# Kernel optimization log

Hardware: AMD Instinct MI355X
Metric: run time of the kernel (lower is better)

## Reference

```python
import jax, jax.numpy as jnp
import numpy as np

EMBED_DIM = 256
NUM_HEADS = 8
NB = 8          # number of scenes (batches)
LQ = 256        # queries per scene
LS = 4096       # source points per scene
LN_EPS = 1e-5


def setup_inputs() -> dict:
    key = jax.random.key(0)
    ks = jax.random.split(key, 8)
    d = EMBED_DIM
    n_q, n_s = NB * LQ, NB * LS
    w_scale = d ** -0.5  # xavier-ish
    return {
        "source": jax.random.normal(ks[0], (n_s, d), jnp.float32),
        "query": jax.random.normal(ks[1], (n_q, d), jnp.float32),
        "source_pe": 0.1 * jax.random.normal(ks[2], (n_s, d), jnp.float32),
        "query_pe": 0.1 * jax.random.normal(ks[3], (n_q, d), jnp.float32),
        "in_proj_w": w_scale * jax.random.normal(ks[4], (3 * d, d), jnp.float32),
        "in_proj_b": jnp.zeros((3 * d,), jnp.float32),
        "out_w": w_scale * jax.random.normal(ks[5], (d, d), jnp.float32),
        "out_b": jnp.zeros((d,), jnp.float32),
        "ln_w": jnp.ones((d,), jnp.float32),
        "ln_b": jnp.zeros((d,), jnp.float32),
        # sorted equal-size segments: token i belongs to scene i // L
        "source_batch": (jnp.arange(n_s, dtype=jnp.int32) // LS).astype(jnp.int32),
        "query_batch": (jnp.arange(n_q, dtype=jnp.int32) // LQ).astype(jnp.int32),
        "B": NB,
    }


def reference(source, query, source_pe, query_pe, in_proj_w, in_proj_b,
              out_w, out_b, ln_w, ln_b, source_batch, query_batch, B):
    d = source.shape[-1]
    H = NUM_HEADS
    hd = d // H
    Lq = query.shape[0] // B
    Ls = source.shape[0] // B

    # batch ids are sorted equal segments -> per-scene gather == reshape
    q_in = (query + query_pe).reshape(B, Lq, d)   # q with pos embed
    k_in = (source + source_pe).reshape(B, Ls, d) # k with pos embed
    v_in = source.reshape(B, Ls, d)               # v without pos embed

    Wq, Wk, Wv = jnp.split(in_proj_w, 3, axis=0)
    bq, bk, bv = jnp.split(in_proj_b, 3)

    q = (q_in @ Wq.T + bq).reshape(B, Lq, H, hd)
    k = (k_in @ Wk.T + bk).reshape(B, Ls, H, hd)
    v = (v_in @ Wv.T + bv).reshape(B, Ls, H, hd)

    scores = jnp.einsum('bqhd,bkhd->bhqk', q, k) * (hd ** -0.5)
    attn = jax.nn.softmax(scores, axis=-1)
    o = jnp.einsum('bhqk,bkhd->bqhd', attn, v).reshape(B, Lq, d)
    o = o @ out_w.T + out_b

    # residual (dropout is identity at p=0) + LayerNorm
    res = o + query.reshape(B, Lq, d)
    mu = jnp.mean(res, axis=-1, keepdims=True)
    var = jnp.var(res, axis=-1, keepdims=True)
    y = (res - mu) * jax.lax.rsqrt(var + LN_EPS) * ln_w + ln_b
    return y.reshape(-1, d)
```

## Files before the change

### kernel.cpp

```cpp
#include <hip/hip_runtime.h>
#include <hip/hip_bf16.h>

typedef __bf16 bf16;
typedef __bf16 bf16x4 __attribute__((ext_vector_type(4)));
typedef __bf16 bf16x8 __attribute__((ext_vector_type(8)));
typedef float f32x4 __attribute__((ext_vector_type(4)));

#define D 256
#define NHEAD 8
#define HD 32
#define NB_ 8
#define LQ_ 256
#define LS_ 4096
#define MQ (NB_ * LQ_)
#define MS (NB_ * LS_)

#define QSCALE 0.25500527f

__global__ __launch_bounds__(256) void prep(
    const float* __restrict__ source, const float* __restrict__ source_pe,
    const float* __restrict__ query, const float* __restrict__ query_pe,
    const float* __restrict__ w_in, const float* __restrict__ w_out,
    bf16* __restrict__ SPb, bf16* __restrict__ Sb, bf16* __restrict__ QPb,
    bf16* __restrict__ Wb, int write_sb)
{
    const int NS4 = MS * D / 4;
    const int NQ4 = MQ * D / 4;
    const int NW4 = (768 * 256 + 256 * 256) / 4;
    const int total = NS4 + NQ4 + NW4;
    for (int i = blockIdx.x * 256 + threadIdx.x; i < total; i += gridDim.x * 256) {
        if (i < NS4) {
            const float4 s = ((const float4*)source)[i];
            const float4 p = ((const float4*)source_pe)[i];
            bf16x4 osp;
            osp[0] = (bf16)(s.x + p.x); osp[1] = (bf16)(s.y + p.y);
            osp[2] = (bf16)(s.z + p.z); osp[3] = (bf16)(s.w + p.w);
            ((bf16x4*)SPb)[i] = osp;
            if (write_sb) {
                bf16x4 os;
                os[0] = (bf16)s.x; os[1] = (bf16)s.y;
                os[2] = (bf16)s.z; os[3] = (bf16)s.w;
                ((bf16x4*)Sb)[i] = os;
            }
        } else if (i < NS4 + NQ4) {
            const int j = i - NS4;
            const float4 s = ((const float4*)query)[j];
            const float4 p = ((const float4*)query_pe)[j];
            bf16x4 o;
            o[0] = (bf16)(s.x + p.x); o[1] = (bf16)(s.y + p.y);
            o[2] = (bf16)(s.z + p.z); o[3] = (bf16)(s.w + p.w);
            ((bf16x4*)QPb)[j] = o;
        } else {
            const int j = i - NS4 - NQ4;
            const float4 v = (j < 49152) ? ((const float4*)w_in)[j]
                                         : ((const float4*)w_out)[j - 49152];
            bf16x4 o;
            o[0] = (bf16)v.x; o[1] = (bf16)v.y; o[2] = (bf16)v.z; o[3] = (bf16)v.w;
            ((bf16x4*)Wb)[j] = o;
        }
    }
}

__global__ __launch_bounds__(256) void prep2(
    const float* __restrict__ source, bf16* __restrict__ Sb)
{
    const int NS4 = MS * D / 4;
    for (int i = blockIdx.x * 256 + threadIdx.x; i < NS4; i += gridDim.x * 256) {
        const float4 s = ((const float4*)source)[i];
        bf16x4 o;
        o[0] = (bf16)s.x; o[1] = (bf16)s.y; o[2] = (bf16)s.z; o[3] = (bf16)s.w;
        ((bf16x4*)Sb)[i] = o;
    }
}

__global__ __launch_bounds__(256, 2) void gemm_proj_all(
    const bf16* __restrict__ SPb, const bf16* __restrict__ Sb,
    const bf16* __restrict__ QPb, const bf16* __restrict__ Wb,
    const float* __restrict__ in_proj_b,
    bf16* __restrict__ Kt, bf16* __restrict__ Vt2, bf16* __restrict__ Qb,
    int mode)
{
    __shared__ bf16 As[128][72];
    __shared__ bf16 Bs[256][72];
    const int tid = threadIdx.x, lane = tid & 63, wid = tid >> 6;
    const int wm = wid >> 1, wn = wid & 1;
    const int g = lane >> 4, q15 = lane & 15;
    const int id = blockIdx.x;

    const bf16* A; const bf16* W; const float* bias; bf16* out;
    int omode; int mblk;
    if (mode == 0) {
        if (id < 256)      { A = SPb; W = Wb + 256 * D; bias = in_proj_b + 256; out = Kt;  mblk = id;       omode = 1; }
        else if (id < 512) { A = Sb;  W = Wb + 512 * D; bias = in_proj_b + 512; out = Vt2; mblk = id - 256; omode = 2; }
        else               { A = QPb; W = Wb;           bias = in_proj_b;       out = Qb;  mblk = id - 512; omode = 0; }
    } else if (mode == 1) {
        if (id < 256)      { A = SPb; W = Wb + 256 * D; bias = in_proj_b + 256; out = Kt;  mblk = id;       omode = 1; }
        else               { A = QPb; W = Wb;           bias = in_proj_b;       out = Qb;  mblk = id - 256; omode = 0; }
    } else {
        A = Sb; W = Wb + 512 * D; bias = in_proj_b + 512; out = Vt2; mblk = id; omode = 2;
    }

    f32x4 acc[4][8];
    #pragma unroll
    for (int i = 0; i < 4; ++i)
        #pragma unroll
        for (int j = 0; j < 8; ++j) acc[i][j] = (f32x4){0.f, 0.f, 0.f, 0.f};

    const size_t arow0 = (size_t)mblk * 128;

    for (int kk = 0; kk < 4; ++kk) {
        const int d0 = kk * 64;
        #pragma unroll
        for (int i = 0; i < 4; ++i) {
            const int idx = i * 256 + tid;
            const int r = idx >> 3, c = (idx & 7) * 8;
            *(bf16x8*)&As[r][c] = *(const bf16x8*)&A[(arow0 + r) * D + d0 + c];
        }
        #pragma unroll
        for (int i = 0; i < 8; ++i) {
            const int idx = i * 256 + tid;
            const int r = idx >> 3, c = (idx & 7) * 8;
            *(bf16x8*)&Bs[r][c] = *(const bf16x8*)&W[(size_t)r * D + d0 + c];
        }
        __syncthreads();
        #pragma unroll
        for (int h2 = 0; h2 < 2; ++h2) {
            const int ko = h2 * 32 + g * 8;
            bf16x8 af[4], bfr[8];
            #pragma unroll
            for (int i = 0; i < 4; ++i)
                af[i] = *(const bf16x8*)&As[wm * 64 + i * 16 + q15][ko];
            #pragma unroll
            for (int j = 0; j < 8; ++j)
                bfr[j] = *(const bf16x8*)&Bs[wn * 128 + j * 16 + q15][ko];
            #pragma unroll
            for (int i = 0; i < 4; ++i)
                #pragma unroll
                for (int j = 0; j < 8; ++j)
                    acc[i][j] = __builtin_amdgcn_mfma_f32_16x16x32_bf16(
                        af[i], bfr[j], acc[i][j], 0, 0, 0);
        }
        __syncthreads();
    }

    if (omode == 0) {
        #pragma unroll
        for (int i = 0; i < 4; ++i)
            #pragma unroll
            for (int j = 0; j < 8; ++j) {
                const int n_g = wn * 128 + j * 16 + q15;
                const float b = bias[n_g];
                #pragma unroll
                for (int r = 0; r < 4; ++r) {
                    const size_t m_g = arow0 + wm * 64 + i * 16 + g * 4 + r;
                    out[m_g * D + n_g] = (bf16)((acc[i][j][r] + b) * QSCALE);
                }
            }
    } else if (omode == 1) {
        #pragma unroll
        for (int i = 0; i < 4; ++i)
            #pragma unroll
            for (int j = 0; j < 8; ++j) {
                const int n_g = wn * 128 + j * 16 + q15;
                const int h = n_g >> 5, d = n_g & 31;
                const int gp = d >> 3, e = d & 7;
                const float b = bias[n_g];
                #pragma unroll
                for (int r = 0; r < 4; ++r) {
                    const size_t m_g = arow0 + wm * 64 + i * 16 + g * 4 + r;
                    const int bb = (int)(m_g >> 12);
                    const int c = (int)((m_g & 4095) >> 6);
                    const int kl = (int)(m_g & 63);
                    const int t = ((kl >> 5) << 1) | ((kl >> 2) & 1);
                    const int q15p = ((kl >> 3) & 3) * 4 + (kl & 3);
                    out[((size_t)(bb * 8 + h) * 64 + c) * 2048
                        + t * 512 + (gp * 16 + q15p) * 8 + e] = (bf16)(acc[i][j][r] + b);
                }
            }
    } else {
        #pragma unroll
        for (int i = 0; i < 4; ++i)
            #pragma unroll
            for (int j = 0; j < 8; ++j) {
                const int n_g = wn * 128 + j * 16 + q15;
                const int h = n_g >> 5, d = n_g & 31;
                const int dt = d >> 4, q15p = d & 15;
                const float b = bias[n_g];
                const size_t m_g0 = arow0 + wm * 64 + i * 16 + g * 4;
                const int bb = (int)(m_g0 >> 12);
                const int c = (int)((m_g0 & 4095) >> 6);
                const int kl0 = (int)(m_g0 & 63);
                const int half = kl0 >> 5, gp = (kl0 >> 3) & 3, e0 = kl0 & 7;
                const int f = dt * 2 + half;
                bf16x4 o;
                #pragma unroll
                for (int r = 0; r < 4; ++r) o[r] = (bf16)(acc[i][j][r] + b);
                *(bf16x4*)&out[((size_t)(bb * 8 + h) * 64 + c) * 2048
                               + f * 512 + (gp * 16 + q15p) * 8 + e0] = o;
            }
    }
}

template<int S>
__global__ __launch_bounds__(256, 8) void attn_kernel(
    const bf16* __restrict__ Qb, const bf16* __restrict__ Kt,
    const bf16* __restrict__ Vt2,
    float* __restrict__ accp, float* __restrict__ lp)
{
    const int tid = threadIdx.x, lane = tid & 63, wid = tid >> 6;
    const int q15 = lane & 15, g = lane >> 4;
    const int bid = blockIdx.x;
    const int h = bid & 7;
    const int inner = bid >> 3;
    const int b = inner / (S * 4);
    const int rem = inner % (S * 4);
    const int split = rem >> 2, qt = rem & 3;
    constexpr int CHUNKS = LS_ / S / 64;

    const int q0 = b * LQ_ + qt * 64 + wid * 16;
    const bf16x8 qf = *(const bf16x8*)&Qb[(size_t)(q0 + q15) * D + h * HD + g * 8];

    const f32x4 minit = (f32x4){-8.f, -8.f, -8.f, -8.f};
    const size_t cbase = ((size_t)(b * 8 + h) * 64 + split * CHUNKS) * 2048;
    const bf16* kp = Kt + cbase + lane * 8;
    const bf16* vp = Vt2 + cbase + lane * 8;

    float l_run = 0.f;
    f32x4 acc0 = (f32x4){0.f, 0.f, 0.f, 0.f};
    f32x4 acc1 = (f32x4){0.f, 0.f, 0.f, 0.f};

    for (int kc = 0; kc < CHUNKS; ++kc) {
        const size_t co = (size_t)kc * 2048;

        bf16x8 kf[4], vf[4];
        #pragma unroll
        for (int t = 0; t < 4; ++t) kf[t] = *(const bf16x8*)&kp[co + t * 512];
        #pragma unroll
        for (int f = 0; f < 4; ++f) vf[f] = *(const bf16x8*)&vp[co + f * 512];

        f32x4 s[4];
        #pragma unroll
        for (int t = 0; t < 4; ++t)
            s[t] = __builtin_amdgcn_mfma_f32_16x16x32_bf16(kf[t], qf, minit, 0, 0, 0);

        bf16x8 pa0, pa1;
        #pragma unroll
        for (int r = 0; r < 4; ++r) {
            const float p0 = exp2f(s[0][r]);
            const float p1 = exp2f(s[1][r]);
            const float p2 = exp2f(s[2][r]);
            const float p3 = exp2f(s[3][r]);
            l_run += (p0 + p1) + (p2 + p3);
            pa0[r]     = (bf16)p0;
            pa0[4 + r] = (bf16)p1;
            pa1[r]     = (bf16)p2;
            pa1[4 + r] = (bf16)p3;
        }

        acc0 = __builtin_amdgcn_mfma_f32_16x16x32_bf16(pa0, vf[0], acc0, 0, 0, 0);
        acc0 = __builtin_amdgcn_mfma_f32_16x16x32_bf16(pa1, vf[1], acc0, 0, 0, 0);
        acc1 = __builtin_amdgcn_mfma_f32_16x16x32_bf16(pa0, vf[2], acc1, 0, 0, 0);
        acc1 = __builtin_amdgcn_mfma_f32_16x16x32_bf16(pa1, vf[3], acc1, 0, 0, 0);
    }

    l_run += __shfl_xor(l_run, 16);
    l_run += __shfl_xor(l_run, 32);

    const int task = (b * 8 + h) * 16 + qt * 4 + wid;
    const size_t base = ((size_t)(task * S + split) * 64 + lane) * 8;
    *(f32x4*)&accp[base]     = acc0;
    *(f32x4*)&accp[base + 4] = acc1;
    if (lane < 16)
        lp[(task * S + split) * 16 + lane] = l_run;
}

template<int S>
__global__ __launch_bounds__(256) void attn_combine(
    const float* __restrict__ accp, const float* __restrict__ lp,
    bf16* __restrict__ Ob)
{
    const int tid = threadIdx.x, lane = tid & 63, wid = tid >> 6;
    const int task = blockIdx.x * 4 + wid;
    const int g = lane >> 4, q15 = lane & 15;

    f32x4 o0 = (f32x4){0.f, 0.f, 0.f, 0.f};
    f32x4 o1 = (f32x4){0.f, 0.f, 0.f, 0.f};
    float ll = 0.f;
    #pragma unroll
    for (int s = 0; s < S; ++s) {
        const size_t base = ((size_t)(task * S + s) * 64 + lane) * 8;
        o0 += *(const f32x4*)&accp[base];
        o1 += *(const f32x4*)&accp[base + 4];
        if (lane < 16) ll += lp[(task * S + s) * 16 + lane];
    }

    const int b = task >> 7, h = (task >> 4) & 7, qg = task & 15;
    #pragma unroll
    for (int r = 0; r < 4; ++r) {
        const float inv = 1.f / __shfl(ll, g * 4 + r);
        const size_t row = (size_t)b * LQ_ + qg * 16 + g * 4 + r;
        Ob[row * D + h * HD + q15]      = (bf16)(o0[r] * inv);
        Ob[row * D + h * HD + 16 + q15] = (bf16)(o1[r] * inv);
    }
}

__global__ __launch_bounds__(256) void out_ln_kernel(
    const bf16* __restrict__ Ob, const bf16* __restrict__ Wout,
    const float* __restrict__ out_b, const float* __restrict__ query,
    const float* __restrict__ lnw, const float* __restrict__ lnb,
    float* __restrict__ out)
{
    __shared__ bf16 As[128][72];
    __shared__ bf16 Bs[256][72];
    __shared__ float red[2][128][2];
    const int tid = threadIdx.x, lane = tid & 63, wid = tid >> 6;
    const int wm = wid >> 1, wn = wid & 1;
    const int g = lane >> 4, q15 = lane & 15;
    const int mblk = blockIdx.x;

    f32x4 acc[4][8];
    #pragma unroll
    for (int i = 0; i < 4; ++i)
        #pragma unroll
        for (int j = 0; j < 8; ++j) acc[i][j] = (f32x4){0.f, 0.f, 0.f, 0.f};

    for (int kk = 0; kk < 4; ++kk) {
        const int d0 = kk * 64;
        #pragma unroll
        for (int i = 0; i < 4; ++i) {
            const int idx = i * 256 + tid;
            const int r = idx >> 3, c = (idx & 7) * 8;
            *(bf16x8*)&As[r][c] =
                *(const bf16x8*)&Ob[(size_t)(mblk * 128 + r) * D + d0 + c];
        }
        #pragma unroll
        for (int i = 0; i < 8; ++i) {
            const int idx = i * 256 + tid;
            const int r = idx >> 3, c = (idx & 7) * 8;
            *(bf16x8*)&Bs[r][c] = *(const bf16x8*)&Wout[(size_t)r * D + d0 + c];
        }
        __syncthreads();
        #pragma unroll
        for (int h2 = 0; h2 < 2; ++h2) {
            const int ko = h2 * 32 + g * 8;
            bf16x8 af[4], bfr[8];
            #pragma unroll
            for (int i = 0; i < 4; ++i)
                af[i] = *(const bf16x8*)&As[wm * 64 + i * 16 + q15][ko];
            #pragma unroll
            for (int j = 0; j < 8; ++j)
                bfr[j] = *(const bf16x8*)&Bs[wn * 128 + j * 16 + q15][ko];
            #pragma unroll
            for (int i = 0; i < 4; ++i)
                #pragma unroll
                for (int j = 0; j < 8; ++j)
                    acc[i][j] = __builtin_amdgcn_mfma_f32_16x16x32_bf16(
                        af[i], bfr[j], acc[i][j], 0, 0, 0);
        }
        __syncthreads();
    }

    float bl[8], lw[8], lbv[8];
    #pragma unroll
    for (int j = 0; j < 8; ++j) {
        const int n = wn * 128 + j * 16 + q15;
        bl[j] = out_b[n]; lw[j] = lnw[n]; lbv[j] = lnb[n];
    }

    #pragma unroll
    for (int i = 0; i < 4; ++i) {
        #pragma unroll
        for (int r = 0; r < 4; ++r) {
            const size_t m = (size_t)mblk * 128 + wm * 64 + i * 16 + g * 4 + r;
            float s = 0.f, sq = 0.f;
            #pragma unroll
            for (int j = 0; j < 8; ++j) {
                const float v = acc[i][j][r] + bl[j] + query[m * D + wn * 128 + j * 16 + q15];
                acc[i][j][r] = v;
                s += v; sq += v * v;
            }
            s += __shfl_xor(s, 1);  sq += __shfl_xor(sq, 1);
            s += __shfl_xor(s, 2);  sq += __shfl_xor(sq, 2);
            s += __shfl_xor(s, 4);  sq += __shfl_xor(sq, 4);
            s += __shfl_xor(s, 8);  sq += __shfl_xor(sq, 8);
            if (q15 == i * 4 + r) {
                red[wn][wm * 64 + i * 16 + g * 4 + r][0] = s;
                red[wn][wm * 64 + i * 16 + g * 4 + r][1] = sq;
            }
        }
    }
    __syncthreads();

    #pragma unroll
    for (int i = 0; i < 4; ++i)
        #pragma unroll
        for (int r = 0; r < 4; ++r) {
            const int row = wm * 64 + i * 16 + g * 4 + r;
            const float s  = red[0][row][0] + red[1][row][0];
            const float sq = red[0][row][1] + red[1][row][1];
            const float mean = s * (1.f / 256.f);
            const float var  = sq * (1.f / 256.f) - mean * mean;
            const float inv  = rsqrtf(var + 1e-5f);
            const size_t m = (size_t)mblk * 128 + row;
            #pragma unroll
            for (int j = 0; j < 8; ++j)
                out[m * D + wn * 128 + j * 16 + q15] =
                    (acc[i][j][r] - mean) * inv * lw[j] + lbv[j];
        }
}

extern "C" void kernel_launch(void* const* d_in, const int* in_sizes, int n_in,
                              void* d_out, int out_size, void* d_ws, size_t ws_size,
                              hipStream_t stream) {
    (void)in_sizes; (void)n_in; (void)out_size;
    const float* source    = (const float*)d_in[0];
    const float* query     = (const float*)d_in[1];
    const float* source_pe = (const float*)d_in[2];
    const float* query_pe  = (const float*)d_in[3];
    const float* in_proj_w = (const float*)d_in[4];
    const float* in_proj_b = (const float*)d_in[5];
    const float* out_w     = (const float*)d_in[6];
    const float* out_b     = (const float*)d_in[7];
    const float* ln_w      = (const float*)d_in[8];
    const float* ln_b      = (const float*)d_in[9];

    constexpr int S = 8;
    bf16* Wb  = (bf16*)d_ws;
    bf16* Qb  = Wb + 1024 * 256;
    bf16* Kt  = Qb + (size_t)MQ * D;
    bf16* Vt2 = Kt + (size_t)MS * D;
    bf16* Ob  = Vt2 + (size_t)MS * D;
    bf16* QPb = Ob + (size_t)MQ * D;
    bf16* SPb = QPb + (size_t)MQ * D;
    bf16* Sb  = SPb + (size_t)MS * D;
    float* lp   = (float*)QPb;
    float* outp = (float*)d_out;

    const size_t need_fast = (size_t)((char*)(Sb + (size_t)MS * D) - (char*)d_ws);
    const bool fast = (ws_size >= need_fast);

    if (fast) {
        prep<<<dim3(2048), dim3(256), 0, stream>>>(
            source, source_pe, query, query_pe, in_proj_w, out_w,
            SPb, Sb, QPb, Wb, 1);
        gemm_proj_all<<<dim3(528), dim3(256), 0, stream>>>(
            SPb, Sb, QPb, Wb, in_proj_b, Kt, Vt2, Qb, 0);
        float* accp = (float*)Sb;
        attn_kernel<S><<<dim3(256 * S), dim3(256), 0, stream>>>(Qb, Kt, Vt2, accp, lp);
        attn_combine<S><<<dim3(256), dim3(256), 0, stream>>>(accp, lp, Ob);
    } else {
        prep<<<dim3(2048), dim3(256), 0, stream>>>(
            source, source_pe, query, query_pe, in_proj_w, out_w,
            SPb, SPb, QPb, Wb, 0);
        gemm_proj_all<<<dim3(272), dim3(256), 0, stream>>>(
            SPb, SPb, QPb, Wb, in_proj_b, Kt, Vt2, Qb, 1);
        prep2<<<dim3(2048), dim3(256), 0, stream>>>(source, SPb);
        gemm_proj_all<<<dim3(256), dim3(256), 0, stream>>>(
            SPb, SPb, QPb, Wb, in_proj_b, Kt, Vt2, Qb, 2);
        float* accp = (float*)SPb;
        attn_kernel<S><<<dim3(256 * S), dim3(256), 0, stream>>>(Qb, Kt, Vt2, accp, lp);
        attn_combine<S><<<dim3(256), dim3(256), 0, stream>>>(accp, lp, Ob);
    }

    out_ln_kernel<<<dim3(16), dim3(256), 0, stream>>>(
        Ob, Wb + 768 * 256, out_b, query, ln_w, ln_b, outp);
}
```

Baseline: 94.42 us.

## Fuse fp32-to-bf16 input conversion into projection GEMM; double queries per attention wave

Removes the standalone prep pass that wrote bf16 copies of source+pe, source and query+pe. The projection GEMM now loads fp32 inputs directly, adds the positional embedding and converts to bf16 while filling shared memory. Only the weights are still cast in a small separate kernel. The attention kernel now has each wave handle 32 queries (two 16-row tiles) that share the same K/V fragment loads, halving the grid and lowering the occupancy hint from 8 to 4. This trades extra register pressure and doubled fp32 global reads inside the GEMM for much less intermediate traffic and better K/V reuse.

```diff
diff --git a/kernel.cpp b/kernel.cpp
--- a/kernel.cpp
+++ b/kernel.cpp
@@ -17,68 +17,25 @@
 
 #define QSCALE 0.25500527f
 
-__global__ __launch_bounds__(256) void prep(
+__global__ __launch_bounds__(256) void wcast(
+    const float* __restrict__ w_in, const float* __restrict__ w_out,
+    bf16* __restrict__ wb)
+{
+    const int idx = blockIdx.x * 256 + threadIdx.x;
+    const int n_in4 = (768 * 256) / 4;
+    float4 v;
+    if (idx < n_in4) v = ((const float4*)w_in)[idx];
+    else             v = ((const float4*)w_out)[idx - n_in4];
+    bf16x4 o;
+    o[0] = (bf16)v.x; o[1] = (bf16)v.y; o[2] = (bf16)v.z; o[3] = (bf16)v.w;
+    *(bf16x4*)&wb[(size_t)idx * 4] = o;
+}
+
+__global__ __launch_bounds__(256, 2) void gemm_fused(
     const float* __restrict__ source, const float* __restrict__ source_pe,
     const float* __restrict__ query, const float* __restrict__ query_pe,
-    const float* __restrict__ w_in, const float* __restrict__ w_out,
-    bf16* __restrict__ SPb, bf16* __restrict__ Sb, bf16* __restrict__ QPb,
-    bf16* __restrict__ Wb, int write_sb)
-{
-    const int NS4 = MS * D / 4;
-    const int NQ4 = MQ * D / 4;
-    const int NW4 = (768 * 256 + 256 * 256) / 4;
-    const int total = NS4 + NQ4 + NW4;
-    for (int i = blockIdx.x * 256 + threadIdx.x; i < total; i += gridDim.x * 256) {
-        if (i < NS4) {
-            const float4 s = ((const float4*)source)[i];
-            const float4 p = ((const float4*)source_pe)[i];
-            bf16x4 osp;
-            osp[0] = (bf16)(s.x + p.x); osp[1] = (bf16)(s.y + p.y);
-            osp[2] = (bf16)(s.z + p.z); osp[3] = (bf16)(s.w + p.w);
-            ((bf16x4*)SPb)[i] = osp;
-            if (write_sb) {
-                bf16x4 os;
-                os[0] = (bf16)s.x; os[1] = (bf16)s.y;
-                os[2] = (bf16)s.z; os[3] = (bf16)s.w;
-                ((bf16x4*)Sb)[i] = os;
-            }
-        } else if (i < NS4 + NQ4) {
-            const int j = i - NS4;
-            const float4 s = ((const float4*)query)[j];
-            const float4 p = ((const float4*)query_pe)[j];
-            bf16x4 o;
-            o[0] = (bf16)(s.x + p.x); o[1] = (bf16)(s.y + p.y);
-            o[2] = (bf16)(s.z + p.z); o[3] = (bf16)(s.w + p.w);
-            ((bf16x4*)QPb)[j] = o;
-        } else {
-            const int j = i - NS4 - NQ4;
-            const float4 v = (j < 49152) ? ((const float4*)w_in)[j]
-                                         : ((const float4*)w_out)[j - 49152];
-            bf16x4 o;
-            o[0] = (bf16)v.x; o[1] = (bf16)v.y; o[2] = (bf16)v.z; o[3] = (bf16)v.w;
-            ((bf16x4*)Wb)[j] = o;
-        }
-    }
-}
-
-__global__ __launch_bounds__(256) void prep2(
-    const float* __restrict__ source, bf16* __restrict__ Sb)
-{
-    const int NS4 = MS * D / 4;
-    for (int i = blockIdx.x * 256 + threadIdx.x; i < NS4; i += gridDim.x * 256) {
-        const float4 s = ((const float4*)source)[i];
-        bf16x4 o;
-        o[0] = (bf16)s.x; o[1] = (bf16)s.y; o[2] = (bf16)s.z; o[3] = (bf16)s.w;
-        ((bf16x4*)Sb)[i] = o;
-    }
-}
-
-__global__ __launch_bounds__(256, 2) void gemm_proj_all(
-    const bf16* __restrict__ SPb, const bf16* __restrict__ Sb,
-    const bf16* __restrict__ QPb, const bf16* __restrict__ Wb,
-    const float* __restrict__ in_proj_b,
-    bf16* __restrict__ Kt, bf16* __restrict__ Vt2, bf16* __restrict__ Qb,
-    int mode)
+    const bf16* __restrict__ Wb, const float* __restrict__ in_proj_b,
+    bf16* __restrict__ Kt, bf16* __restrict__ Vt2, bf16* __restrict__ Qb)
 {
     __shared__ bf16 As[128][72];
     __shared__ bf16 Bs[256][72];
@@ -87,17 +44,17 @@
     const int g = lane >> 4, q15 = lane & 15;
     const int id = blockIdx.x;
 
-    const bf16* A; const bf16* W; const float* bias; bf16* out;
+    const float* A; const float* P; const bf16* W; const float* bias; bf16* out;
     int omode; int mblk;
-    if (mode == 0) {
-        if (id < 256)      { A = SPb; W = Wb + 256 * D; bias = in_proj_b + 256; out = Kt;  mblk = id;       omode = 1; }
-        else if (id < 512) { A = Sb;  W = Wb + 512 * D; bias = in_proj_b + 512; out = Vt2; mblk = id - 256; omode = 2; }
-        else               { A = QPb; W = Wb;           bias = in_proj_b;       out = Qb;  mblk = id - 512; omode = 0; }
-    } else if (mode == 1) {
-        if (id < 256)      { A = SPb; W = Wb + 256 * D; bias = in_proj_b + 256; out = Kt;  mblk = id;       omode = 1; }
-        else               { A = QPb; W = Wb;           bias = in_proj_b;       out = Qb;  mblk = id - 256; omode = 0; }
+    if (id < 256) {
+        A = source; P = source_pe; W = Wb + 256 * D; bias = in_proj_b + 256;
+        out = Kt; mblk = id; omode = 1;
+    } else if (id < 512) {
+        A = source; P = nullptr;   W = Wb + 512 * D; bias = in_proj_b + 512;
+        out = Vt2; mblk = id - 256; omode = 2;
     } else {
-        A = Sb; W = Wb + 512 * D; bias = in_proj_b + 512; out = Vt2; mblk = id; omode = 2;
+        A = query;  P = query_pe;  W = Wb;           bias = in_proj_b;
+        out = Qb; mblk = id - 512; omode = 0;
     }
 
     f32x4 acc[4][8];
@@ -111,10 +68,18 @@
     for (int kk = 0; kk < 4; ++kk) {
         const int d0 = kk * 64;
         #pragma unroll
-        for (int i = 0; i < 4; ++i) {
+        for (int i = 0; i < 8; ++i) {
             const int idx = i * 256 + tid;
-            const int r = idx >> 3, c = (idx & 7) * 8;
-            *(bf16x8*)&As[r][c] = *(const bf16x8*)&A[(arow0 + r) * D + d0 + c];
+            const int r = idx >> 4, c = (idx & 15) * 4;
+            const size_t gof = (arow0 + r) * D + d0 + c;
+            float4 v = *(const float4*)&A[gof];
+            if (P) {
+                const float4 p = *(const float4*)&P[gof];
+                v.x += p.x; v.y += p.y; v.z += p.z; v.w += p.w;
+            }
+            bf16x4 o;
+            o[0] = (bf16)v.x; o[1] = (bf16)v.y; o[2] = (bf16)v.z; o[3] = (bf16)v.w;
+            *(bf16x4*)&As[r][c] = o;
         }
         #pragma unroll
         for (int i = 0; i < 8; ++i) {
@@ -202,7 +167,7 @@
 }
 
 template<int S>
-__global__ __launch_bounds__(256, 8) void attn_kernel(
+__global__ __launch_bounds__(256, 4) void attn_kernel(
     const bf16* __restrict__ Qb, const bf16* __restrict__ Kt,
     const bf16* __restrict__ Vt2,
     float* __restrict__ accp, float* __restrict__ lp)
@@ -212,22 +177,26 @@
     const int bid = blockIdx.x;
     const int h = bid & 7;
     const int inner = bid >> 3;
-    const int b = inner / (S * 4);
-    const int rem = inner % (S * 4);
-    const int split = rem >> 2, qt = rem & 3;
+    const int split = inner % S;
+    const int tmp = inner / S;
+    const int qt = tmp & 1;
+    const int b = tmp >> 1;
     constexpr int CHUNKS = LS_ / S / 64;
 
-    const int q0 = b * LQ_ + qt * 64 + wid * 16;
-    const bf16x8 qf = *(const bf16x8*)&Qb[(size_t)(q0 + q15) * D + h * HD + g * 8];
+    const int q0 = b * LQ_ + qt * 128 + wid * 32;
+    const bf16x8 qfA = *(const bf16x8*)&Qb[(size_t)(q0 + q15) * D + h * HD + g * 8];
+    const bf16x8 qfB = *(const bf16x8*)&Qb[(size_t)(q0 + 16 + q15) * D + h * HD + g * 8];
 
     const f32x4 minit = (f32x4){-8.f, -8.f, -8.f, -8.f};
     const size_t cbase = ((size_t)(b * 8 + h) * 64 + split * CHUNKS) * 2048;
     const bf16* kp = Kt + cbase + lane * 8;
     const bf16* vp = Vt2 + cbase + lane * 8;
 
-    float l_run = 0.f;
-    f32x4 acc0 = (f32x4){0.f, 0.f, 0.f, 0.f};
-    f32x4 acc1 = (f32x4){0.f, 0.f, 0.f, 0.f};
+    float lA = 0.f, lB = 0.f;
+    f32x4 accA0 = (f32x4){0.f, 0.f, 0.f, 0.f};
+    f32x4 accA1 = (f32x4){0.f, 0.f, 0.f, 0.f};
+    f32x4 accB0 = (f32x4){0.f, 0.f, 0.f, 0.f};
+    f32x4 accB1 = (f32x4){0.f, 0.f, 0.f, 0.f};
 
     for (int kc = 0; kc < CHUNKS; ++kc) {
         const size_t co = (size_t)kc * 2048;
@@ -238,40 +207,60 @@
         #pragma unroll
         for (int f = 0; f < 4; ++f) vf[f] = *(const bf16x8*)&vp[co + f * 512];
 
-        f32x4 s[4];
+        f32x4 sA[4], sB[4];
         #pragma unroll
         for (int t = 0; t < 4; ++t)
-            s[t] = __builtin_amdgcn_mfma_f32_16x16x32_bf16(kf[t], qf, minit, 0, 0, 0);
-
-        bf16x8 pa0, pa1;
+            sA[t] = __builtin_amdgcn_mfma_f32_16x16x32_bf16(kf[t], qfA, minit, 0, 0, 0);
+        #pragma unroll
+        for (int t = 0; t < 4; ++t)
+            sB[t] = __builtin_amdgcn_mfma_f32_16x16x32_bf16(kf[t], qfB, minit, 0, 0, 0);
+
+        bf16x8 paA0, paA1, paB0, paB1;
         #pragma unroll
         for (int r = 0; r < 4; ++r) {
-            const float p0 = exp2f(s[0][r]);
-            const float p1 = exp2f(s[1][r]);
-            const float p2 = exp2f(s[2][r]);
-            const float p3 = exp2f(s[3][r]);
-            l_run += (p0 + p1) + (p2 + p3);
-            pa0[r]     = (bf16)p0;
-            pa0[4 + r] = (bf16)p1;
-            pa1[r]     = (bf16)p2;
-            pa1[4 + r] = (bf16)p3;
-        }
-
-        acc0 = __builtin_amdgcn_mfma_f32_16x16x32_bf16(pa0, vf[0], acc0, 0, 0, 0);
-        acc0 = __builtin_amdgcn_mfma_f32_16x16x32_bf16(pa1, vf[1], acc0, 0, 0, 0);
-        acc1 = __builtin_amdgcn_mfma_f32_16x16x32_bf16(pa0, vf[2], acc1, 0, 0, 0);
-        acc1 = __builtin_amdgcn_mfma_f32_16x16x32_bf16(pa1, vf[3], acc1, 0, 0, 0);
-    }
-
-    l_run += __shfl_xor(l_run, 16);
-    l_run += __shfl_xor(l_run, 32);
-
-    const int task = (b * 8 + h) * 16 + qt * 4 + wid;
-    const size_t base = ((size_t)(task * S + split) * 64 + lane) * 8;
-    *(f32x4*)&accp[base]     = acc0;
-    *(f32x4*)&accp[base + 4] = acc1;
-    if (lane < 16)
-        lp[(task * S + split) * 16 + lane] = l_run;
+            const float a0 = exp2f(sA[0][r]);
+            const float a1 = exp2f(sA[1][r]);
+            const float a2 = exp2f(sA[2][r]);
+            const float a3 = exp2f(sA[3][r]);
+            lA += (a0 + a1) + (a2 + a3);
+            paA0[r] = (bf16)a0; paA0[4 + r] = (bf16)a1;
+            paA1[r] = (bf16)a2; paA1[4 + r] = (bf16)a3;
+            const float b0 = exp2f(sB[0][r]);
+            const float b1 = exp2f(sB[1][r]);
+            const float b2 = exp2f(sB[2][r]);
+            const float b3 = exp2f(sB[3][r]);
+            lB += (b0 + b1) + (b2 + b3);
+            paB0[r] = (bf16)b0; paB0[4 + r] = (bf16)b1;
+            paB1[r] = (bf16)b2; paB1[4 + r] = (bf16)b3;
+        }
+
+        accA0 = __builtin_amdgcn_mfma_f32_16x16x32_bf16(paA0, vf[0], accA0, 0, 0, 0);
+        accA0 = __builtin_amdgcn_mfma_f32_16x16x32_bf16(paA1, vf[1], accA0, 0, 0, 0);
+        accA1 = __builtin_amdgcn_mfma_f32_16x16x32_bf16(paA0, vf[2], accA1, 0, 0, 0);
+        accA1 = __builtin_amdgcn_mfma_f32_16x16x32_bf16(paA1, vf[3], accA1, 0, 0, 0);
+        accB0 = __builtin_amdgcn_mfma_f32_16x16x32_bf16(paB0, vf[0], accB0, 0, 0, 0);
+        accB0 = __builtin_amdgcn_mfma_f32_16x16x32_bf16(paB1, vf[1], accB0, 0, 0, 0);
+        accB1 = __builtin_amdgcn_mfma_f32_16x16x32_bf16(paB0, vf[2], accB1, 0, 0, 0);
+        accB1 = __builtin_amdgcn_mfma_f32_16x16x32_bf16(paB1, vf[3], accB1, 0, 0, 0);
+    }
+
+    lA += __shfl_xor(lA, 16);
+    lA += __shfl_xor(lA, 32);
+    lB += __shfl_xor(lB, 16);
+    lB += __shfl_xor(lB, 32);
+
+    const int qg16 = qt * 8 + wid * 2;
+    const int taskA = (b * 8 + h) * 16 + qg16;
+    const size_t baseA = ((size_t)(taskA * S + split) * 64 + lane) * 8;
+    *(f32x4*)&accp[baseA]     = accA0;
+    *(f32x4*)&accp[baseA + 4] = accA1;
+    const size_t baseB = ((size_t)((taskA + 1) * S + split) * 64 + lane) * 8;
+    *(f32x4*)&accp[baseB]     = accB0;
+    *(f32x4*)&accp[baseB + 4] = accB1;
+    if (lane < 16) {
+        lp[(taskA * S + split) * 16 + lane] = lA;
+        lp[((taskA + 1) * S + split) * 16 + lane] = lB;
+    }
 }
 
 template<int S>
@@ -412,7 +401,7 @@
 extern "C" void kernel_launch(void* const* d_in, const int* in_sizes, int n_in,
                               void* d_out, int out_size, void* d_ws, size_t ws_size,
                               hipStream_t stream) {
-    (void)in_sizes; (void)n_in; (void)out_size;
+    (void)in_sizes; (void)n_in; (void)out_size; (void)ws_size;
     const float* source    = (const float*)d_in[0];
     const float* query     = (const float*)d_in[1];
     const float* source_pe = (const float*)d_in[2];
@@ -430,38 +419,15 @@
     bf16* Kt  = Qb + (size_t)MQ * D;
     bf16* Vt2 = Kt + (size_t)MS * D;
     bf16* Ob  = Vt2 + (size_t)MS * D;
-    bf16* QPb = Ob + (size_t)MQ * D;
-    bf16* SPb = QPb + (size_t)MQ * D;
-    bf16* Sb  = SPb + (size_t)MS * D;
-    float* lp   = (float*)QPb;
+    float* lp = (float*)(Ob + (size_t)MQ * D);
+    float* accp = lp + (size_t)1024 * S * 16;
     float* outp = (float*)d_out;
 
-    const size_t need_fast = (size_t)((char*)(Sb + (size_t)MS * D) - (char*)d_ws);
-    const bool fast = (ws_size >= need_fast);
-
-    if (fast) {
-        prep<<<dim3(2048), dim3(256), 0, stream>>>(
-            source, source_pe, query, query_pe, in_proj_w, out_w,
-            SPb, Sb, QPb, Wb, 1);
-        gemm_proj_all<<<dim3(528), dim3(256), 0, stream>>>(
-            SPb, Sb, QPb, Wb, in_proj_b, Kt, Vt2, Qb, 0);
-        float* accp = (float*)Sb;
-        attn_kernel<S><<<dim3(256 * S), dim3(256), 0, stream>>>(Qb, Kt, Vt2, accp, lp);
-        attn_combine<S><<<dim3(256), dim3(256), 0, stream>>>(accp, lp, Ob);
-    } else {
-        prep<<<dim3(2048), dim3(256), 0, stream>>>(
-            source, source_pe, query, query_pe, in_proj_w, out_w,
-            SPb, SPb, QPb, Wb, 0);
-        gemm_proj_all<<<dim3(272), dim3(256), 0, stream>>>(
-            SPb, SPb, QPb, Wb, in_proj_b, Kt, Vt2, Qb, 1);
-        prep2<<<dim3(2048), dim3(256), 0, stream>>>(source, SPb);
-        gemm_proj_all<<<dim3(256), dim3(256), 0, stream>>>(
-            SPb, SPb, QPb, Wb, in_proj_b, Kt, Vt2, Qb, 2);
-        float* accp = (float*)SPb;
-        attn_kernel<S><<<dim3(256 * S), dim3(256), 0, stream>>>(Qb, Kt, Vt2, accp, lp);
-        attn_combine<S><<<dim3(256), dim3(256), 0, stream>>>(accp, lp, Ob);
-    }
-
+    wcast<<<dim3(256), dim3(256), 0, stream>>>(in_proj_w, out_w, Wb);
+    gemm_fused<<<dim3(528), dim3(256), 0, stream>>>(
+        source, source_pe, query, query_pe, Wb, in_proj_b, Kt, Vt2, Qb);
+    attn_kernel<S><<<dim3(1024), dim3(256), 0, stream>>>(Qb, Kt, Vt2, accp, lp);
+    attn_combine<S><<<dim3(256), dim3(256), 0, stream>>>(accp, lp, Ob);
     out_ln_kernel<<<dim3(16), dim3(256), 0, stream>>>(
         Ob, Wb + 768 * 256, out_b, query, ln_w, ln_b, outp);
 }
```

Measured after the change: 116.2 us. 1.23x slower.
